# Kernel optimization log

Measured on AMD Instinct MI355X. Metric: run time of the kernel, lower is better.

The kernel has to match this reference:

```python
import jax, jax.numpy as jnp
import numpy as np

B, S, D = 4, 2048, 1024
E, ES, K = 16, 256, 4  # n_experts, expert_size, top-k (= n_heads)
STD_GATE = 0.02


def setup_inputs() -> dict:
    key = jax.random.key(0)
    k1, k2, k3, k4 = jax.random.split(key, 4)
    x = jax.random.normal(k1, (B, S, D), dtype=jnp.float32)
    # init per module: gate ~ N(0, d^-0.5), keys ~ N(0, d^-0.5), values ~ N(0, size^-0.5)
    w_gate = jax.random.normal(k2, (E, D), dtype=jnp.float32) * (D ** -0.5)
    keys = jax.random.normal(k3, (E, D, ES), dtype=jnp.float32) * (D ** -0.5)
    values = jax.random.normal(k4, (E, ES, D), dtype=jnp.float32) * ((E * ES) ** -0.5)
    return {"x": x, "w_gate": w_gate, "keys": keys, "values": values}


def reference(x, w_gate, keys, values):
    # sigma-MoE forward (selection_mode='sigmoid', activation=relu,
    # num_selected = n_heads = K, no bias, no dropout, eval mode)
    xt = x.reshape(-1, D)                         # [T, D]
    T = xt.shape[0]
    logits = xt @ w_gate.T                        # [T, E]
    sel = jax.nn.sigmoid(logits)                  # sigmoid gating
    sel_val, sel_idx = jax.lax.top_k(sel, K)      # [T, K]
    # sparse gate weights as dense [T, E] mask (zeros for unselected experts)
    gate_w = jnp.zeros((T, E), dtype=x.dtype).at[
        jnp.arange(T)[:, None], sel_idx
    ].set(sel_val)
    # per-expert hidden: h[t,e,s] = relu(sum_d x[t,d] keys[e,d,s])
    h = jax.nn.relu(jnp.einsum('td,eds->tes', xt, keys))  # [T, E, ES]
    # weighted scatter back through values: out = sum_e gate * h_e @ values_e
    out = jnp.einsum('tes,te,esv->tv', h, gate_w, values)  # [T, D]
    return out.reshape(B, S, D)
```

## Files before the change

kernel.cpp:

```cpp
#include <hip/hip_runtime.h>
#include <hip/hip_bf16.h>
#include <stdint.h>

#define T_TOK 8192
#define DIM   1024
#define NEXP  16
#define ESZ   256
#define TOPK  4
#define BM    64
#define BK    64
#define NPAIR (T_TOK*TOPK)
#define NGB   (T_TOK/4)
#define NBLK  128
#define MAXROWS (NPAIR + NEXP*BM)
#define MAXTILES (NPAIR/BM + NEXP)

typedef __hip_bfloat16 bf16;
typedef short bf16x8 __attribute__((ext_vector_type(8)));
typedef float f32x4 __attribute__((ext_vector_type(4)));

__device__ __forceinline__ unsigned short f2bu(float f){
  __hip_bfloat16 b = __float2bfloat16(f);
  return *reinterpret_cast<unsigned short*>(&b);
}
__device__ __forceinline__ float bu2f(unsigned short u){
  __hip_bfloat16 b = *reinterpret_cast<__hip_bfloat16*>(&u);
  return __bfloat162float(b);
}

__device__ __forceinline__ void gload16(const void* g, void* l){
  __builtin_amdgcn_global_load_lds((const __attribute__((address_space(1))) void*)g,
                                   (__attribute__((address_space(3))) void*)l, 16, 0, 0);
}

__global__ __launch_bounds__(256) void k_gate(const float* __restrict__ x,
    const float* __restrict__ wg, bf16* __restrict__ xb,
    int* __restrict__ sel_idx, float* __restrict__ sel_gate,
    int* __restrict__ block_hist)
{
  __shared__ int h[NEXP];
  if (threadIdx.x < NEXP) h[threadIdx.x] = 0;
  __syncthreads();

  const int wave = threadIdx.x >> 6, lane = threadIdx.x & 63;
  const int t = blockIdx.x*4 + wave;
  const float* xr = x + (size_t)t*DIM;
  float4 xv[4];
#pragma unroll
  for (int c=0;c<4;c++) xv[c] = *(const float4*)(xr + c*256 + lane*4);
#pragma unroll
  for (int c=0;c<4;c++){
    ushort4 o; o.x=f2bu(xv[c].x); o.y=f2bu(xv[c].y); o.z=f2bu(xv[c].z); o.w=f2bu(xv[c].w);
    *(ushort4*)((unsigned short*)xb + (size_t)t*DIM + c*256 + lane*4) = o;
  }
  float sg[NEXP];
#pragma unroll
  for (int e=0;e<NEXP;e++){
    const float* wr = wg + e*DIM;
    float p = 0.f;
#pragma unroll
    for (int c=0;c<4;c++){
      float4 w = *(const float4*)(wr + c*256 + lane*4);
      p += xv[c].x*w.x + xv[c].y*w.y + xv[c].z*w.z + xv[c].w*w.w;
    }
#pragma unroll
    for (int s=1;s<64;s<<=1) p += __shfl_xor(p, s);
    sg[e] = 1.f/(1.f + expf(-p));
  }
  if (lane==0){
    unsigned chosen = 0;
#pragma unroll
    for (int k=0;k<TOPK;k++){
      float best=-1.f; int bi=0;
#pragma unroll
      for (int e=0;e<NEXP;e++){
        float v = ((chosen>>e)&1u) ? -2.f : sg[e];
        if (v>best){best=v;bi=e;}
      }
      chosen |= 1u<<bi;
      sel_idx[t*TOPK+k]=bi; sel_gate[t*TOPK+k]=best;
      atomicAdd(&h[bi], 1);
    }
  }
  __syncthreads();
  if (threadIdx.x < NEXP) block_hist[blockIdx.x*NEXP + threadIdx.x] = h[threadIdx.x];
}

__global__ __launch_bounds__(256) void k_transpose2(const float* __restrict__ keys,
    const float* __restrict__ values, bf16* __restrict__ kT, bf16* __restrict__ vT)
{
  __shared__ float tile[32][33];
  const int which = blockIdx.y >> 4, e = blockIdx.y & 15;
  const int R = which ? ESZ : DIM, C = which ? DIM : ESZ;
  const float* src = (which ? values : keys) + (size_t)e*DIM*ESZ;
  bf16* dst = (which ? vT : kT) + (size_t)e*DIM*ESZ;
  const int ctiles = C/32;
  const int r0 = (blockIdx.x / ctiles)*32, c0 = (blockIdx.x % ctiles)*32;
  const int tx = threadIdx.x & 31, ty = threadIdx.x >> 5;
#pragma unroll
  for (int i=0;i<4;i++){ int r = ty + i*8; tile[r][tx] = src[(size_t)(r0+r)*C + c0 + tx]; }
  __syncthreads();
#pragma unroll
  for (int i=0;i<4;i++){ int r = ty + i*8; dst[(size_t)(c0+r)*R + r0 + tx] = __float2bfloat16(tile[tx][r]); }
}

__global__ void k_meta(const int* __restrict__ gh,
    int* __restrict__ tile_expert, int* __restrict__ tile_rowstart,
    int* __restrict__ tile_segend, int* __restrict__ block_base)
{
  __shared__ int sbc[NBLK][NEXP];
  __shared__ int cnt[NEXP], seg[NEXP];
  const int tid = threadIdx.x;
  for (int cell = tid; cell < NBLK*NEXP; cell += 256){
    int sb = cell >> 4, e = cell & 15;
    int s = 0;
#pragma unroll
    for (int g=0; g<16; ++g) s += gh[(sb*16+g)*NEXP + e];
    sbc[sb][e] = s;
  }
  __syncthreads();
  if (tid < NEXP){
    int s=0;
    for (int sb=0; sb<NBLK; sb++) s += sbc[sb][tid];
    cnt[tid]=s;
  }
  __syncthreads();
  if (tid==0){
    int off=0, tc=0;
    for (int e=0;e<NEXP;e++){
      seg[e]=off;
      int c = cnt[e];
      int nt = (c + BM - 1)/BM;
      for (int i=0;i<nt;i++){
        tile_expert[tc]=e; tile_rowstart[tc]=off+i*BM; tile_segend[tc]=off+c; tc++;
      }
      off += nt*BM;
    }
    for (; tc<MAXTILES; tc++) tile_expert[tc]=-1;
  }
  __syncthreads();
  if (tid < NEXP){
    int s = seg[tid];
    for (int sb=0; sb<NBLK; sb++){ block_base[sb*NEXP + tid] = s; s += sbc[sb][tid]; }
  }
}

__global__ __launch_bounds__(256) void k_scatter(const int* __restrict__ sel_idx,
    const float* __restrict__ sel_gate, const int* __restrict__ block_base,
    int* __restrict__ assign_token, float* __restrict__ assign_gate,
    int* __restrict__ inv_rows)
{
  __shared__ int wcnt[4][NEXP];
  const int p = blockIdx.x*256 + threadIdx.x;
  const int wave = threadIdx.x >> 6, lane = threadIdx.x & 63;
  const int e = sel_idx[p];
  const float g = sel_gate[p];
  int rank = 0;
#pragma unroll
  for (int ee=0; ee<NEXP; ee++){
    unsigned long long m = __ballot(e==ee);
    if (lane==0) wcnt[wave][ee] = (int)__popcll(m);
    if (e==ee) rank = (int)__popcll(m & ((1ull<<lane)-1ull));
  }
  __syncthreads();
  int pre = 0;
  for (int w=0; w<wave; w++) pre += wcnt[w][e];
  const int row = block_base[blockIdx.x*NEXP + e] + pre + rank;
  assign_token[row] = p >> 2;
  assign_gate[row]  = g;
  inv_rows[p] = row;
}

__global__ __launch_bounds__(256) void k_gemm1(
    const bf16* __restrict__ xb, const bf16* __restrict__ kT,
    const int* __restrict__ assign_token, const float* __restrict__ assign_gate,
    const int* __restrict__ tile_expert, const int* __restrict__ tile_rowstart,
    const int* __restrict__ tile_segend, bf16* __restrict__ h)
{
  __shared__ char smem[49152];
  __shared__ int   tokens_s[BM];
  __shared__ float gates_s[BM];

  const int nb = blockIdx.x, tile = blockIdx.y;
  const int e = tile_expert[tile];
  if (e < 0) return;
  const int row0 = tile_rowstart[tile];
  const int segend = tile_segend[tile];
  const int tid = threadIdx.x, wave = tid>>6, lane = tid&63;

  if (tid < BM){
    int rg = row0 + tid;
    bool vld = rg < segend;
    tokens_s[tid] = vld ? assign_token[rg] : 0;
    gates_s[tid]  = vld ? assign_gate[rg] : 0.f;
  }
  __syncthreads();

  const bf16* qA[2]; const bf16* qB[4]; int loA[2], loB[4];
#pragma unroll
  for (int i=0;i<2;i++){
    int row = i*32 + wave*8 + (lane>>3);
    int c   = (lane&7) ^ (row&7);
    qA[i] = xb + (size_t)tokens_s[row]*DIM + c*8;
    loA[i] = i*4096 + wave*1024;
  }
#pragma unroll
  for (int i=0;i<4;i++){
    int col = i*32 + wave*8 + (lane>>3);
    int c   = (lane&7) ^ (col&7);
    qB[i] = kT + ((size_t)e*ESZ + nb*128 + col)*DIM + c*8;
    loB[i] = i*4096 + wave*1024;
  }

  const int wr0 = (wave>>1)*32, wc0 = (wave&1)*64;
  int offA[2][2], offB[2][4];
#pragma unroll
  for (int kk=0;kk<2;kk++){
    int kb = kk*64 + (lane>>4)*16;
#pragma unroll
    for (int m=0;m<2;m++){ int row = wr0 + m*16 + (lane&15); offA[kk][m] = row*128 + (kb ^ ((row&7)<<4)); }
#pragma unroll
    for (int n=0;n<4;n++){ int col = wc0 + n*16 + (lane&15); offB[kk][n] = col*128 + (kb ^ ((col&7)<<4)); }
  }

  f32x4 acc[2][4];
#pragma unroll
  for (int m=0;m<2;m++)
#pragma unroll
    for (int n=0;n<4;n++) acc[m][n] = {0.f,0.f,0.f,0.f};

  auto stage = [&](int abase, int bbase){
#pragma unroll
    for (int i=0;i<2;i++){ gload16(qA[i], smem + abase + loA[i]); qA[i]+=BK; }
#pragma unroll
    for (int i=0;i<4;i++){ gload16(qB[i], smem + bbase + loB[i]); qB[i]+=BK; }
  };
  auto compute = [&](const char* Ab, const char* Bb){
#pragma unroll
    for (int kk=0;kk<2;kk++){
      bf16x8 af[2], bfr[4];
#pragma unroll
      for (int m=0;m<2;m++) af[m]  = *(const bf16x8*)(Ab + offA[kk][m]);
#pragma unroll
      for (int n=0;n<4;n++) bfr[n] = *(const bf16x8*)(Bb + offB[kk][n]);
#pragma unroll
      for (int m=0;m<2;m++)
#pragma unroll
        for (int n=0;n<4;n++)
          acc[m][n] = __builtin_amdgcn_mfma_f32_16x16x32_bf16(af[m], bfr[n], acc[m][n], 0,0,0);
    }
  };

  stage(0, 16384);
  asm volatile("s_waitcnt vmcnt(0)" ::: "memory");
  __builtin_amdgcn_s_barrier();

  for (int kt=0; kt<16; kt+=2){
    stage(8192, 32768);
    compute(smem, smem+16384);
    asm volatile("s_waitcnt vmcnt(0)" ::: "memory");
    __builtin_amdgcn_s_barrier();
    if (kt+2 < 16) stage(0, 16384);
    compute(smem+8192, smem+32768);
    asm volatile("s_waitcnt vmcnt(0)" ::: "memory");
    __builtin_amdgcn_s_barrier();
  }

#pragma unroll
  for (int m=0;m<2;m++)
#pragma unroll
    for (int n=0;n<4;n++){
      int col = wc0 + n*16 + (lane&15);
#pragma unroll
      for (int j=0;j<4;j++){
        int rloc = wr0 + m*16 + ((lane>>4)<<2) + j;
        float v = fmaxf(acc[m][n][j], 0.f) * gates_s[rloc];
        h[(size_t)(row0 + rloc)*ESZ + nb*128 + col] = __float2bfloat16(v);
      }
    }
}

__global__ __launch_bounds__(256) void k_gemm2(
    const bf16* __restrict__ h, const bf16* __restrict__ vT,
    const int* __restrict__ tile_expert, const int* __restrict__ tile_rowstart,
    bf16* __restrict__ partial)
{
  __shared__ char smem[49152];

  const int nb = blockIdx.x, tile = blockIdx.y;
  const int e = tile_expert[tile];
  if (e < 0) return;
  const int row0 = tile_rowstart[tile];
  const int tid = threadIdx.x, wave = tid>>6, lane = tid&63;

  const bf16* qA[2]; const bf16* qB[4]; int loA[2], loB[4];
#pragma unroll
  for (int i=0;i<2;i++){
    int row = i*32 + wave*8 + (lane>>3);
    int c   = (lane&7) ^ (row&7);
    qA[i] = h + (size_t)(row0 + row)*ESZ + c*8;
    loA[i] = i*4096 + wave*1024;
  }
#pragma unroll
  for (int i=0;i<4;i++){
    int col = i*32 + wave*8 + (lane>>3);
    int c   = (lane&7) ^ (col&7);
    qB[i] = vT + ((size_t)e*DIM + nb*128 + col)*ESZ + c*8;
    loB[i] = i*4096 + wave*1024;
  }

  const int wr0 = (wave>>1)*32, wc0 = (wave&1)*64;
  int offA[2][2], offB[2][4];
#pragma unroll
  for (int kk=0;kk<2;kk++){
    int kb = kk*64 + (lane>>4)*16;
#pragma unroll
    for (int m=0;m<2;m++){ int row = wr0 + m*16 + (lane&15); offA[kk][m] = row*128 + (kb ^ ((row&7)<<4)); }
#pragma unroll
    for (int n=0;n<4;n++){ int col = wc0 + n*16 + (lane&15); offB[kk][n] = col*128 + (kb ^ ((col&7)<<4)); }
  }

  f32x4 acc[2][4];
#pragma unroll
  for (int m=0;m<2;m++)
#pragma unroll
    for (int n=0;n<4;n++) acc[m][n] = {0.f,0.f,0.f,0.f};

  auto stage = [&](int abase, int bbase){
#pragma unroll
    for (int i=0;i<2;i++){ gload16(qA[i], smem + abase + loA[i]); qA[i]+=BK; }
#pragma unroll
    for (int i=0;i<4;i++){ gload16(qB[i], smem + bbase + loB[i]); qB[i]+=BK; }
  };
  auto compute = [&](const char* Ab, const char* Bb){
#pragma unroll
    for (int kk=0;kk<2;kk++){
      bf16x8 af[2], bfr[4];
#pragma unroll
      for (int m=0;m<2;m++) af[m]  = *(const bf16x8*)(Ab + offA[kk][m]);
#pragma unroll
      for (int n=0;n<4;n++) bfr[n] = *(const bf16x8*)(Bb + offB[kk][n]);
#pragma unroll
      for (int m=0;m<2;m++)
#pragma unroll
        for (int n=0;n<4;n++)
          acc[m][n] = __builtin_amdgcn_mfma_f32_16x16x32_bf16(af[m], bfr[n], acc[m][n], 0,0,0);
    }
  };

  stage(0, 16384);
  asm volatile("s_waitcnt vmcnt(0)" ::: "memory");
  __builtin_amdgcn_s_barrier();

  stage(8192, 32768);
  compute(smem, smem+16384);
  asm volatile("s_waitcnt vmcnt(0)" ::: "memory");
  __builtin_amdgcn_s_barrier();
  stage(0, 16384);
  compute(smem+8192, smem+32768);
  asm volatile("s_waitcnt vmcnt(0)" ::: "memory");
  __builtin_amdgcn_s_barrier();
  stage(8192, 32768);
  compute(smem, smem+16384);
  asm volatile("s_waitcnt vmcnt(0)" ::: "memory");
  __builtin_amdgcn_s_barrier();
  compute(smem+8192, smem+32768);

#pragma unroll
  for (int m=0;m<2;m++)
#pragma unroll
    for (int n=0;n<4;n++){
      int col = wc0 + n*16 + (lane&15);
#pragma unroll
      for (int j=0;j<4;j++){
        int rloc = wr0 + m*16 + ((lane>>4)<<2) + j;
        partial[(size_t)(row0 + rloc)*DIM + nb*128 + col] = __float2bfloat16(acc[m][n][j]);
      }
    }
}

__global__ __launch_bounds__(256) void k_reduce(const bf16* __restrict__ partial,
    const int* __restrict__ inv_rows, float* __restrict__ out)
{
  const int t = blockIdx.x;
  const int c0 = threadIdx.x * 4;
  int rows[TOPK];
#pragma unroll
  for (int k=0;k<TOPK;k++) rows[k] = inv_rows[t*TOPK+k];
  float a0=0.f,a1=0.f,a2=0.f,a3=0.f;
#pragma unroll
  for (int k=0;k<TOPK;k++){
    ushort4 v = *(const ushort4*)((const unsigned short*)partial + (size_t)rows[k]*DIM + c0);
    a0 += bu2f(v.x); a1 += bu2f(v.y); a2 += bu2f(v.z); a3 += bu2f(v.w);
  }
  float4 o = {a0,a1,a2,a3};
  *(float4*)(out + (size_t)t*DIM + c0) = o;
}

extern "C" void kernel_launch(void* const* d_in, const int* in_sizes, int n_in,
                              void* d_out, int out_size, void* d_ws, size_t ws_size,
                              hipStream_t stream)
{
  const float* x      = (const float*)d_in[0];
  const float* wg     = (const float*)d_in[1];
  const float* keys   = (const float*)d_in[2];
  const float* values = (const float*)d_in[3];
  float* out = (float*)d_out;

  char* ws = (char*)d_ws;
  size_t off = 0;
  bf16* vT   = (bf16*)(ws+off); off += (size_t)NEXP*DIM*ESZ*2;
  bf16* hbuf = (bf16*)(ws+off); off += (size_t)MAXROWS*ESZ*2;
  int*   sel_idx      = (int*)  (ws+off); off += (size_t)NPAIR*4;
  float* sel_gate     = (float*)(ws+off); off += (size_t)NPAIR*4;
  int*   assign_token = (int*)  (ws+off); off += (size_t)MAXROWS*4;
  float* assign_gate  = (float*)(ws+off); off += (size_t)MAXROWS*4;
  int*   inv_rows     = (int*)  (ws+off); off += (size_t)NPAIR*4;
  int*   block_hist   = (int*)  (ws+off); off += (size_t)NGB*NEXP*4;
  int*   block_base   = (int*)  (ws+off); off += (size_t)NBLK*NEXP*4;
  int*   tile_expert  = (int*)  (ws+off); off += 4096;
  int*   tile_rowstart= (int*)  (ws+off); off += 4096;
  int*   tile_segend  = (int*)  (ws+off); off += 4096;
  const size_t PARTIAL_BYTES = (size_t)MAXROWS*DIM*2;
  const size_t XB_BYTES = (size_t)T_TOK*DIM*2;
  const size_t KT_BYTES = (size_t)NEXP*ESZ*DIM*2;
  bf16* partial = (bf16*)(ws+off); off += PARTIAL_BYTES;
  bf16* xb = (bf16*)((char*)partial + PARTIAL_BYTES - XB_BYTES - KT_BYTES);
  bf16* kT = (bf16*)((char*)partial + PARTIAL_BYTES - KT_BYTES);

  k_gate<<<NGB, 256, 0, stream>>>(x, wg, xb, sel_idx, sel_gate, block_hist);
  k_transpose2<<<dim3(256, NEXP*2), 256, 0, stream>>>(keys, values, kT, vT);
  k_meta<<<1, 256, 0, stream>>>(block_hist, tile_expert, tile_rowstart, tile_segend, block_base);
  k_scatter<<<NBLK, 256, 0, stream>>>(sel_idx, sel_gate, block_base, assign_token,
      assign_gate, inv_rows);
  k_gemm1<<<dim3(2, MAXTILES), 256, 0, stream>>>(xb, kT, assign_token, assign_gate,
      tile_expert, tile_rowstart, tile_segend, hbuf);
  k_gemm2<<<dim3(8, MAXTILES), 256, 0, stream>>>(hbuf, vT,
      tile_expert, tile_rowstart, partial);
  k_reduce<<<T_TOK, 256, 0, stream>>>(partial, inv_rows, out);
}
```

Before: 162.8 us.

## Stage gate weights in LDS and process 16 tokens per gating block

The gating kernel now copies the full 16x1024 gate weight matrix into shared memory once per block and has each block handle 16 tokens instead of 4. Each half-wave processes two tokens at once, reusing the weight loads across them, and reduces with a 32-lane shuffle. Top-k runs redundantly in every lane instead of a single serial lane. The per-block histogram layout shrinks, so the metadata kernel's reduction is adjusted to match. This trades fewer global weight reads for 64KB of LDS per block, which lowers occupancy.

```diff
diff --git a/kernel.cpp b/kernel.cpp
--- a/kernel.cpp
+++ b/kernel.cpp
@@ -10,8 +10,9 @@
 #define BM    64
 #define BK    64
 #define NPAIR (T_TOK*TOPK)
-#define NGB   (T_TOK/4)
+#define NGB   (T_TOK/16)
 #define NBLK  128
+#define GPB   (NGB/NBLK)
 #define MAXROWS (NPAIR + NEXP*BM)
 #define MAXTILES (NPAIR/BM + NEXP)
 
@@ -38,49 +39,76 @@
     int* __restrict__ sel_idx, float* __restrict__ sel_gate,
     int* __restrict__ block_hist)
 {
+  __shared__ float wlds[NEXP*DIM];
   __shared__ int h[NEXP];
+  {
+    const float4* src = (const float4*)wg;
+    float4* dst = (float4*)wlds;
+#pragma unroll
+    for (int i=0;i<16;i++) dst[threadIdx.x + i*256] = src[threadIdx.x + i*256];
+  }
   if (threadIdx.x < NEXP) h[threadIdx.x] = 0;
   __syncthreads();
 
-  const int wave = threadIdx.x >> 6, lane = threadIdx.x & 63;
-  const int t = blockIdx.x*4 + wave;
-  const float* xr = x + (size_t)t*DIM;
-  float4 xv[4];
-#pragma unroll
-  for (int c=0;c<4;c++) xv[c] = *(const float4*)(xr + c*256 + lane*4);
-#pragma unroll
-  for (int c=0;c<4;c++){
-    ushort4 o; o.x=f2bu(xv[c].x); o.y=f2bu(xv[c].y); o.z=f2bu(xv[c].z); o.w=f2bu(xv[c].w);
-    *(ushort4*)((unsigned short*)xb + (size_t)t*DIM + c*256 + lane*4) = o;
-  }
-  float sg[NEXP];
+  const int ts = threadIdx.x >> 5;
+  const int dc = threadIdx.x & 31;
+  const int t0 = blockIdx.x*16 + ts;
+  const int t1 = t0 + 8;
+  const float* xr0 = x + (size_t)t0*DIM;
+  const float* xr1 = x + (size_t)t1*DIM;
+  unsigned short* xb0 = (unsigned short*)xb + (size_t)t0*DIM;
+  unsigned short* xb1 = (unsigned short*)xb + (size_t)t1*DIM;
+
+  float acc0[NEXP], acc1[NEXP];
+#pragma unroll
+  for (int e=0;e<NEXP;e++){ acc0[e]=0.f; acc1[e]=0.f; }
+
+#pragma unroll
+  for (int i=0;i<8;i++){
+    const int d0 = i*128 + dc*4;
+    float4 xv0 = *(const float4*)(xr0 + d0);
+    float4 xv1 = *(const float4*)(xr1 + d0);
+    ushort4 o0; o0.x=f2bu(xv0.x); o0.y=f2bu(xv0.y); o0.z=f2bu(xv0.z); o0.w=f2bu(xv0.w);
+    ushort4 o1; o1.x=f2bu(xv1.x); o1.y=f2bu(xv1.y); o1.z=f2bu(xv1.z); o1.w=f2bu(xv1.w);
+    *(ushort4*)(xb0 + d0) = o0;
+    *(ushort4*)(xb1 + d0) = o1;
+#pragma unroll
+    for (int e=0;e<NEXP;e++){
+      float2 wa = *(const float2*)(wlds + e*DIM + d0);
+      float2 wb = *(const float2*)(wlds + e*DIM + d0 + 2);
+      acc0[e] += xv0.x*wa.x + xv0.y*wa.y + xv0.z*wb.x + xv0.w*wb.y;
+      acc1[e] += xv1.x*wa.x + xv1.y*wa.y + xv1.z*wb.x + xv1.w*wb.y;
+    }
+  }
+
 #pragma unroll
   for (int e=0;e<NEXP;e++){
-    const float* wr = wg + e*DIM;
-    float p = 0.f;
-#pragma unroll
-    for (int c=0;c<4;c++){
-      float4 w = *(const float4*)(wr + c*256 + lane*4);
-      p += xv[c].x*w.x + xv[c].y*w.y + xv[c].z*w.z + xv[c].w*w.w;
-    }
-#pragma unroll
-    for (int s=1;s<64;s<<=1) p += __shfl_xor(p, s);
-    sg[e] = 1.f/(1.f + expf(-p));
-  }
-  if (lane==0){
-    unsigned chosen = 0;
-#pragma unroll
-    for (int k=0;k<TOPK;k++){
-      float best=-1.f; int bi=0;
-#pragma unroll
-      for (int e=0;e<NEXP;e++){
-        float v = ((chosen>>e)&1u) ? -2.f : sg[e];
-        if (v>best){best=v;bi=e;}
-      }
-      chosen |= 1u<<bi;
-      sel_idx[t*TOPK+k]=bi; sel_gate[t*TOPK+k]=best;
-      atomicAdd(&h[bi], 1);
-    }
+#pragma unroll
+    for (int s=1;s<32;s<<=1){
+      acc0[e] += __shfl_xor(acc0[e], s);
+      acc1[e] += __shfl_xor(acc1[e], s);
+    }
+  }
+
+#pragma unroll
+  for (int e=0;e<NEXP;e++){
+    acc0[e] = 1.f/(1.f + expf(-acc0[e]));
+    acc1[e] = 1.f/(1.f + expf(-acc1[e]));
+  }
+#pragma unroll
+  for (int k=0;k<TOPK;k++){
+    float b0=-2.f, b1=-2.f; int i0=0, i1=0;
+#pragma unroll
+    for (int e=0;e<NEXP;e++){
+      if (acc0[e] > b0){ b0=acc0[e]; i0=e; }
+      if (acc1[e] > b1){ b1=acc1[e]; i1=e; }
+    }
+    if (dc==0){
+      sel_idx[t0*TOPK+k]=i0; sel_gate[t0*TOPK+k]=b0;
+      sel_idx[t1*TOPK+k]=i1; sel_gate[t1*TOPK+k]=b1;
+      atomicAdd(&h[i0],1); atomicAdd(&h[i1],1);
+    }
+    acc0[i0] = -2.f; acc1[i1] = -2.f;
   }
   __syncthreads();
   if (threadIdx.x < NEXP) block_hist[blockIdx.x*NEXP + threadIdx.x] = h[threadIdx.x];
@@ -115,7 +143,7 @@
     int sb = cell >> 4, e = cell & 15;
     int s = 0;
 #pragma unroll
-    for (int g=0; g<16; ++g) s += gh[(sb*16+g)*NEXP + e];
+    for (int g=0; g<GPB; ++g) s += gh[(sb*GPB+g)*NEXP + e];
     sbc[sb][e] = s;
   }
   __syncthreads();
```

New measurement: 150.3 us. 7.7% less time.
